# Performance work log

Measured on AMD Instinct MI355X. Metric: run time of the kernel, lower is better.

The kernel has to match this reference:

```python
import jax, jax.numpy as jnp
import numpy as np

N, I, O, G = 16384, 128, 128, 16


def setup_inputs() -> dict:
    key = jax.random.key(0)
    k1, k2, k3 = jax.random.split(key, 3)
    coef_norm = np.sqrt(I) * np.sqrt(G)  # smooth_initialization=False
    return {
        "x": jax.random.normal(k1, (N, I), dtype=jnp.float32),
        "cos_amplitudes": jax.random.normal(k2, (O, I, G), dtype=jnp.float32) / coef_norm,
        "sin_amplitudes": jax.random.normal(k3, (O, I, G), dtype=jnp.float32) / coef_norm,
        "bias": jnp.zeros((O,), dtype=jnp.float32),
        "ln_gamma": jnp.ones((O,), dtype=jnp.float32),
        "ln_beta": jnp.zeros((O,), dtype=jnp.float32),
    }


def reference(x, cos_amplitudes, sin_amplitudes, bias, ln_gamma, ln_beta):
    g = cos_amplitudes.shape[-1]
    # frequencies buffer: init_freq_scale=1.0 -> [1, 2, ..., grid_size]
    freqs = jnp.arange(1, g + 1, dtype=x.dtype)  # (G,)
    phases = x[:, :, None] * freqs               # (N, I, G)
    # contraction expressed as a GEMM instead of broadcast-sum over (N,O,I,G)
    out = jnp.einsum("nig,oig->no", jnp.cos(phases), cos_amplitudes)
    out = out + jnp.einsum("nig,oig->no", jnp.sin(phases), sin_amplitudes)
    out = out + bias  # (N, O)
    # LayerNorm over output_dim, eps=1e-5 (torch default)
    mu = jnp.mean(out, axis=-1, keepdims=True)
    var = jnp.var(out, axis=-1, keepdims=True)
    out = (out - mu) / jnp.sqrt(var + 1e-5) * ln_gamma + ln_beta
    return out
```

## Files before the change

### kernel.cpp

```cpp
#include <hip/hip_runtime.h>
#include <hip/hip_bf16.h>
#include <math.h>

#define N_TOK 16384
#define I_DIM 128
#define O_DIM 128
#define G_DIM 16
#define BN 64
#define CI 4
#define KC (CI * G_DIM * 2)
#define NCHUNK (I_DIM / CI)
#define A_STRIDE 136
#define ABUF (BN * A_STRIDE)
#define C_STRIDE 132

typedef __bf16 bf16x8 __attribute__((ext_vector_type(8)));
typedef float  f32x4  __attribute__((ext_vector_type(4)));

__global__ __launch_bounds__(256) void fkan_pack_b(
    const float* __restrict__ cosA, const float* __restrict__ sinA,
    __bf16* __restrict__ Bp)
{
    int tid = blockIdx.x * 256 + threadIdx.x;
    int gq  = tid & 3;
    int i   = (tid >> 2) & 127;
    int o   = tid >> 9;
    int c   = i >> 2, ks = i & 3;
    int cg  = o >> 5, ot = (o >> 4) & 1, row16 = o & 15;
    int lane = gq * 16 + row16;
    size_t sbase = ((size_t)o * I_DIM + i) * G_DIM + gq * 4;
    float4 cv = *(const float4*)(cosA + sbase);
    float4 sv = *(const float4*)(sinA + sbase);
    bf16x8 v;
    v[0] = (__bf16)cv.x; v[1] = (__bf16)sv.x;
    v[2] = (__bf16)cv.y; v[3] = (__bf16)sv.y;
    v[4] = (__bf16)cv.z; v[5] = (__bf16)sv.z;
    v[6] = (__bf16)cv.w; v[7] = (__bf16)sv.w;
    size_t frag = (((size_t)c * 4 + cg) * 4 + ks) * 2 + ot;
    *(bf16x8*)(Bp + (frag * 64 + lane) * 8) = v;
}

__global__ __launch_bounds__(256) void fkan_main(
    const float* __restrict__ x,
    const __bf16* __restrict__ Bp,
    const float* __restrict__ bias,
    const float* __restrict__ gamma,
    const float* __restrict__ beta,
    float* __restrict__ out)
{
    __shared__ __align__(16) __bf16 smem[2 * ABUF];
    __bf16* A0 = smem;
    __bf16* A1 = smem + ABUF;

    const int t     = threadIdx.x;
    const int lane  = t & 63;
    const int cg    = t >> 6;
    const int row16 = lane & 15;
    const int quad  = lane >> 4;
    const int n0    = blockIdx.x * BN;

    const int fn  = t >> 2;
    const int fil = t & 3;

    f32x4 acc[4][2];
#pragma unroll
    for (int mt = 0; mt < 4; ++mt)
#pragma unroll
        for (int ot = 0; ot < 2; ++ot)
            acc[mt][ot] = (f32x4){0.f, 0.f, 0.f, 0.f};

    bf16x8 bA[2][4], bB[2][4];

    auto ld_x = [&](int c) -> float {
        return x[(size_t)(n0 + fn) * I_DIM + c * CI + fil];
    };

    auto ld_b = [&](int c, bf16x8 (&b)[2][4]) {
        const bf16x8* base = (const bf16x8*)Bp + ((size_t)(c * 4 + cg) * 8) * 64 + lane;
#pragma unroll
        for (int ks = 0; ks < 4; ++ks)
#pragma unroll
            for (int ot = 0; ot < 2; ++ot)
                b[ot][ks] = base[(ks * 2 + ot) * 64];
    };

    auto stage_a = [&](float xv, __bf16* Ab) {
        float s1, c1;
        __sincosf(xv, &s1, &c1);
        __align__(16) __bf16 feat[32];
        feat[0] = (__bf16)c1;
        feat[1] = (__bf16)s1;
        float ck = c1, sk = s1;
#pragma unroll
        for (int g = 1; g < 16; ++g) {
            float cn = ck * c1 - sk * s1;
            float sn = sk * c1 + ck * s1;
            feat[2 * g]     = (__bf16)cn;
            feat[2 * g + 1] = (__bf16)sn;
            ck = cn; sk = sn;
        }
        bf16x8* dst = (bf16x8*)(Ab + fn * A_STRIDE + fil * 32);
        const bf16x8* srcv = (const bf16x8*)feat;
#pragma unroll
        for (int j = 0; j < 4; ++j) dst[j] = srcv[j];
    };

    auto phase = [&](int c, const __bf16* Ar, __bf16* Aw,
                     bf16x8 (&bcur)[2][4], bf16x8 (&bnext)[2][4], float xs, float& xn) {
        const bool pf = (c + 1 < NCHUNK);
        if (pf) ld_b(c + 1, bnext);
        if (c + 2 < NCHUNK) xn = ld_x(c + 2);
        if (pf) stage_a(xs, Aw);

        __builtin_amdgcn_s_setprio(1);
#pragma unroll
        for (int ks = 0; ks < 4; ++ks) {
            bf16x8 a[4];
#pragma unroll
            for (int mt = 0; mt < 4; ++mt)
                a[mt] = *(const bf16x8*)(Ar + (mt * 16 + row16) * A_STRIDE
                                         + ks * 32 + quad * 8);
#pragma unroll
            for (int mt = 0; mt < 4; ++mt) {
                acc[mt][0] = __builtin_amdgcn_mfma_f32_16x16x32_bf16(a[mt], bcur[0][ks], acc[mt][0], 0, 0, 0);
                acc[mt][1] = __builtin_amdgcn_mfma_f32_16x16x32_bf16(a[mt], bcur[1][ks], acc[mt][1], 0, 0, 0);
            }
        }
        __builtin_amdgcn_s_setprio(0);

        asm volatile("s_waitcnt lgkmcnt(0)" ::: "memory");
        __builtin_amdgcn_sched_barrier(0);
        __builtin_amdgcn_s_barrier();
    };

    float xA = ld_x(0);
    float xB;
    ld_b(0, bA);
    stage_a(xA, A0);
    xB = ld_x(1);
    asm volatile("s_waitcnt lgkmcnt(0)" ::: "memory");
    __builtin_amdgcn_s_barrier();

    for (int cc = 0; cc < NCHUNK / 2; ++cc) {
        phase(2 * cc,     A0, A1, bA, bB, xB, xA);
        phase(2 * cc + 1, A1, A0, bB, bA, xA, xB);
    }

    float* Cs = (float*)smem;
#pragma unroll
    for (int mt = 0; mt < 4; ++mt)
#pragma unroll
        for (int ot = 0; ot < 2; ++ot)
#pragma unroll
            for (int r = 0; r < 4; ++r)
                Cs[(mt * 16 + quad * 4 + r) * C_STRIDE + cg * 32 + ot * 16 + row16] =
                    acc[mt][ot][r];
    __syncthreads();

    {
        const int r  = t >> 2;
        const int qt = t & 3;
        const float* crow = Cs + r * C_STRIDE + qt * 32;
        float vals[32];
        float sum = 0.f, sumsq = 0.f;
#pragma unroll
        for (int j4 = 0; j4 < 8; ++j4) {
            f32x4 v4 = *(const f32x4*)(crow + 4 * j4);
#pragma unroll
            for (int e = 0; e < 4; ++e) {
                float v = v4[e] + bias[qt * 32 + 4 * j4 + e];
                vals[4 * j4 + e] = v;
                sum += v;
                sumsq += v * v;
            }
        }
        sum   += __shfl_xor(sum, 1);   sum   += __shfl_xor(sum, 2);
        sumsq += __shfl_xor(sumsq, 1); sumsq += __shfl_xor(sumsq, 2);
        float mu   = sum * (1.0f / O_DIM);
        float var  = sumsq * (1.0f / O_DIM) - mu * mu;
        float rstd = rsqrtf(var + 1e-5f);

        float* orow = out + (size_t)(n0 + r) * O_DIM + qt * 32;
#pragma unroll
        for (int j4 = 0; j4 < 8; ++j4) {
            float4 o4;
            o4.x = (vals[4*j4+0] - mu) * rstd * gamma[qt*32 + 4*j4+0] + beta[qt*32 + 4*j4+0];
            o4.y = (vals[4*j4+1] - mu) * rstd * gamma[qt*32 + 4*j4+1] + beta[qt*32 + 4*j4+1];
            o4.z = (vals[4*j4+2] - mu) * rstd * gamma[qt*32 + 4*j4+2] + beta[qt*32 + 4*j4+2];
            o4.w = (vals[4*j4+3] - mu) * rstd * gamma[qt*32 + 4*j4+3] + beta[qt*32 + 4*j4+3];
            *(float4*)(orow + 4 * j4) = o4;
        }
    }
}

extern "C" void kernel_launch(void* const* d_in, const int* in_sizes, int n_in,
                              void* d_out, int out_size, void* d_ws, size_t ws_size,
                              hipStream_t stream) {
    const float* x     = (const float*)d_in[0];
    const float* cosA  = (const float*)d_in[1];
    const float* sinA  = (const float*)d_in[2];
    const float* bias  = (const float*)d_in[3];
    const float* gamma = (const float*)d_in[4];
    const float* beta  = (const float*)d_in[5];
    float* out = (float*)d_out;

    __bf16* Bp = (__bf16*)d_ws;

    fkan_pack_b<<<dim3((NCHUNK * O_DIM * KC) / 8 / 256), dim3(256), 0, stream>>>(cosA, sinA, Bp);
    fkan_main<<<dim3(N_TOK / BN), dim3(256), 0, stream>>>(x, Bp, bias, gamma, beta, out);
}
```

Baseline: 104.5 us.

## Stage B fragments through LDS via async global_load_lds and coalesce packing

The main kernel now double-buffers B operand fragments in shared memory using direct global-to-LDS loads, instead of prefetching them into registers. This frees VGPRs and overlaps the B transfer with compute through a vmcnt wait. The pack kernel is also restructured to read coalesced rows into LDS before writing the fragments. The cost is a larger LDS footprint, which may lower occupancy, plus extra LDS reads per k-step. The always-issued clamped prefetch loads also add redundant traffic on the last chunks.

```diff
diff --git a/kernel.cpp b/kernel.cpp
--- a/kernel.cpp
+++ b/kernel.cpp
@@ -12,32 +12,59 @@
 #define NCHUNK (I_DIM / CI)
 #define A_STRIDE 136
 #define ABUF (BN * A_STRIDE)
+#define BSLICE 4096
+#define BBUF (4 * BSLICE)
 #define C_STRIDE 132
+#define PK_STRIDE 68
 
 typedef __bf16 bf16x8 __attribute__((ext_vector_type(8)));
 typedef float  f32x4  __attribute__((ext_vector_type(4)));
+
+#define GLOAD_LDS16(g, l) __builtin_amdgcn_global_load_lds( \
+    (const __attribute__((address_space(1))) void*)(g),     \
+    (__attribute__((address_space(3))) void*)(l), 16, 0, 0)
 
 __global__ __launch_bounds__(256) void fkan_pack_b(
     const float* __restrict__ cosA, const float* __restrict__ sinA,
     __bf16* __restrict__ Bp)
 {
-    int tid = blockIdx.x * 256 + threadIdx.x;
-    int gq  = tid & 3;
-    int i   = (tid >> 2) & 127;
-    int o   = tid >> 9;
-    int c   = i >> 2, ks = i & 3;
-    int cg  = o >> 5, ot = (o >> 4) & 1, row16 = o & 15;
-    int lane = gq * 16 + row16;
-    size_t sbase = ((size_t)o * I_DIM + i) * G_DIM + gq * 4;
-    float4 cv = *(const float4*)(cosA + sbase);
-    float4 sv = *(const float4*)(sinA + sbase);
-    bf16x8 v;
-    v[0] = (__bf16)cv.x; v[1] = (__bf16)sv.x;
-    v[2] = (__bf16)cv.y; v[3] = (__bf16)sv.y;
-    v[4] = (__bf16)cv.z; v[5] = (__bf16)sv.z;
-    v[6] = (__bf16)cv.w; v[7] = (__bf16)sv.w;
-    size_t frag = (((size_t)c * 4 + cg) * 4 + ks) * 2 + ot;
-    *(bf16x8*)(Bp + (frag * 64 + lane) * 8) = v;
+    __shared__ __align__(16) float cosL[32 * PK_STRIDE];
+    __shared__ __align__(16) float sinL[32 * PK_STRIDE];
+    const int b = blockIdx.x;
+    const int t = threadIdx.x;
+    const int c = b >> 2, cg = b & 3;
+
+    {
+        const int o_l = t >> 3;
+        const int k   = t & 7;
+        const float* srcc = cosA + ((size_t)(cg * 32 + o_l) * I_DIM + c * 4) * G_DIM;
+        const float* srcs = sinA + ((size_t)(cg * 32 + o_l) * I_DIM + c * 4) * G_DIM;
+#pragma unroll
+        for (int h = 0; h < 2; ++h) {
+            int col = (k + 8 * h) * 4;
+            *(float4*)(cosL + o_l * PK_STRIDE + col) = *(const float4*)(srcc + col);
+            *(float4*)(sinL + o_l * PK_STRIDE + col) = *(const float4*)(srcs + col);
+        }
+    }
+    __syncthreads();
+
+#pragma unroll
+    for (int h = 0; h < 2; ++h) {
+        int gi    = t + 256 * h;
+        int fl    = gi >> 6;
+        int lane  = gi & 63;
+        int ks    = fl >> 1, ot = fl & 1;
+        int row16 = lane & 15, quad = lane >> 4;
+        int orow  = ot * 16 + row16;
+        int colb  = ks * 16 + quad * 4;
+        bf16x8 v;
+#pragma unroll
+        for (int j = 0; j < 4; ++j) {
+            v[2 * j]     = (__bf16)cosL[orow * PK_STRIDE + colb + j];
+            v[2 * j + 1] = (__bf16)sinL[orow * PK_STRIDE + colb + j];
+        }
+        *(bf16x8*)(Bp + ((size_t)b * 512 + gi) * 8) = v;
+    }
 }
 
 __global__ __launch_bounds__(256) void fkan_main(
@@ -48,9 +75,11 @@
     const float* __restrict__ beta,
     float* __restrict__ out)
 {
-    __shared__ __align__(16) __bf16 smem[2 * ABUF];
+    __shared__ __align__(16) __bf16 smem[2 * ABUF + 2 * BBUF];
     __bf16* A0 = smem;
     __bf16* A1 = smem + ABUF;
+    __bf16* B0 = smem + 2 * ABUF;
+    __bf16* B1 = B0 + BBUF;
 
     const int t     = threadIdx.x;
     const int lane  = t & 63;
@@ -69,19 +98,16 @@
         for (int ot = 0; ot < 2; ++ot)
             acc[mt][ot] = (f32x4){0.f, 0.f, 0.f, 0.f};
 
-    bf16x8 bA[2][4], bB[2][4];
-
     auto ld_x = [&](int c) -> float {
         return x[(size_t)(n0 + fn) * I_DIM + c * CI + fil];
     };
 
-    auto ld_b = [&](int c, bf16x8 (&b)[2][4]) {
-        const bf16x8* base = (const bf16x8*)Bp + ((size_t)(c * 4 + cg) * 8) * 64 + lane;
-#pragma unroll
-        for (int ks = 0; ks < 4; ++ks)
-#pragma unroll
-            for (int ot = 0; ot < 2; ++ot)
-                b[ot][ks] = base[(ks * 2 + ot) * 64];
+    auto dma_b = [&](int c, __bf16* Bw) {
+        const __bf16* src = Bp + (size_t)(c * 4 + cg) * 4096 + lane * 8;
+        __bf16* dst = Bw + cg * BSLICE + lane * 8;
+#pragma unroll
+        for (int j = 0; j < 8; ++j)
+            GLOAD_LDS16(src + j * 512, dst + j * 512);
     };
 
     auto stage_a = [&](float xv, __bf16* Ab) {
@@ -106,15 +132,19 @@
     };
 
     auto phase = [&](int c, const __bf16* Ar, __bf16* Aw,
-                     bf16x8 (&bcur)[2][4], bf16x8 (&bnext)[2][4], float xs, float& xn) {
-        const bool pf = (c + 1 < NCHUNK);
-        if (pf) ld_b(c + 1, bnext);
-        if (c + 2 < NCHUNK) xn = ld_x(c + 2);
-        if (pf) stage_a(xs, Aw);
-
+                     const __bf16* Br, __bf16* Bw, float xs, float& xn) {
+        int cx = (c + 2 < NCHUNK) ? c + 2 : NCHUNK - 1;
+        int cb = (c + 1 < NCHUNK) ? c + 1 : NCHUNK - 1;
+        xn = ld_x(cx);
+        dma_b(cb, Bw);
+        stage_a(xs, Aw);
+
+        asm volatile("s_waitcnt vmcnt(9)" ::: "memory");
         __builtin_amdgcn_s_setprio(1);
 #pragma unroll
         for (int ks = 0; ks < 4; ++ks) {
+            bf16x8 b0 = *(const bf16x8*)(Br + cg * BSLICE + (ks * 2 + 0) * 512 + lane * 8);
+            bf16x8 b1 = *(const bf16x8*)(Br + cg * BSLICE + (ks * 2 + 1) * 512 + lane * 8);
             bf16x8 a[4];
 #pragma unroll
             for (int mt = 0; mt < 4; ++mt)
@@ -122,8 +152,8 @@
                                          + ks * 32 + quad * 8);
 #pragma unroll
             for (int mt = 0; mt < 4; ++mt) {
-                acc[mt][0] = __builtin_amdgcn_mfma_f32_16x16x32_bf16(a[mt], bcur[0][ks], acc[mt][0], 0, 0, 0);
-                acc[mt][1] = __builtin_amdgcn_mfma_f32_16x16x32_bf16(a[mt], bcur[1][ks], acc[mt][1], 0, 0, 0);
+                acc[mt][0] = __builtin_amdgcn_mfma_f32_16x16x32_bf16(a[mt], b0, acc[mt][0], 0, 0, 0);
+                acc[mt][1] = __builtin_amdgcn_mfma_f32_16x16x32_bf16(a[mt], b1, acc[mt][1], 0, 0, 0);
             }
         }
         __builtin_amdgcn_s_setprio(0);
@@ -134,16 +164,15 @@
     };
 
     float xA = ld_x(0);
-    float xB;
-    ld_b(0, bA);
+    float xB = ld_x(1);
+    dma_b(0, B0);
     stage_a(xA, A0);
-    xB = ld_x(1);
     asm volatile("s_waitcnt lgkmcnt(0)" ::: "memory");
     __builtin_amdgcn_s_barrier();
 
     for (int cc = 0; cc < NCHUNK / 2; ++cc) {
-        phase(2 * cc,     A0, A1, bA, bB, xB, xA);
-        phase(2 * cc + 1, A1, A0, bB, bA, xA, xB);
+        phase(2 * cc,     A0, A1, B0, B1, xB, xA);
+        phase(2 * cc + 1, A1, A0, B1, B0, xA, xB);
     }
 
     float* Cs = (float*)smem;
@@ -206,6 +235,6 @@
 
     __bf16* Bp = (__bf16*)d_ws;
 
-    fkan_pack_b<<<dim3((NCHUNK * O_DIM * KC) / 8 / 256), dim3(256), 0, stream>>>(cosA, sinA, Bp);
+    fkan_pack_b<<<dim3(128), dim3(256), 0, stream>>>(cosA, sinA, Bp);
     fkan_main<<<dim3(N_TOK / BN), dim3(256), 0, stream>>>(x, Bp, bias, gamma, beta, out);
 }
```

Result: slower. 117.7 us (+12.6%).
